# Optimization experiments

Hardware: AMD Instinct MI355X
Metric: run time of the kernel (lower is better)

## Reference

```python
import jax, jax.numpy as jnp
import numpy as np

B, S, T = 32, 128, 64
H = 512
VS = VT = 32000


def _lstm_cell(x, h, c, W, U, b):
    # Keras LSTM gate order: i, f, g(cell), o
    z = x @ W + h @ U + b
    i, f, g, o = jnp.split(z, 4, axis=-1)
    c = jax.nn.sigmoid(f) * c + jax.nn.sigmoid(i) * jnp.tanh(g)
    h = jax.nn.sigmoid(o) * jnp.tanh(c)
    return h, c


def _lstm_scan(xs, h0, c0, W, U, b):
    # xs: [S, B, D]
    def step(carry, x):
        h, c = _lstm_cell(x, carry[0], carry[1], W, U, b)
        return (h, c), h
    (hT, cT), hs = jax.lax.scan(step, (h0, c0), xs)
    return hs, hT, cT


def setup_inputs() -> dict:
    key = jax.random.key(0)
    ks = jax.random.split(key, 16)
    def n(k, shape, s=0.02):
        return (jax.random.normal(k, shape, jnp.float32) * s).astype(jnp.float32)
    return {
        "src": jax.random.randint(ks[0], (B, S), 0, VS, jnp.int32),
        "trg": jax.random.randint(ks[1], (B, T), 0, VT, jnp.int32),
        "E_src": n(ks[2], (VS, H)),
        "E_trg": n(ks[3], (VT, H)),
        "Wf": n(ks[4], (H, 4 * H)), "Uf": n(ks[5], (H, 4 * H)), "bf": jnp.zeros((4 * H,), jnp.float32),
        "Wb": n(ks[6], (H, 4 * H)), "Ub": n(ks[7], (H, 4 * H)), "bb": jnp.zeros((4 * H,), jnp.float32),
        "Wd": n(ks[8], (H, 4 * H)), "Ud": n(ks[9], (H, 4 * H)), "bd": jnp.zeros((4 * H,), jnp.float32),
        "fcW": n(ks[10], (2 * H, H)), "fcb": jnp.zeros((H,), jnp.float32),
        "clsW": n(ks[11], (2 * H, VT)), "clsb": jnp.zeros((VT,), jnp.float32),
    }


def reference(src, trg, E_src, E_trg, Wf, Uf, bf, Wb, Ub, bb, Wd, Ud, bd, fcW, fcb, clsW, clsb):
    Bn = src.shape[0]
    Hn = E_src.shape[1]
    # --- Encoder: bidirectional LSTM ---
    xs = E_src[src].transpose(1, 0, 2)          # [S, B, H]
    z0 = jnp.zeros((Bn, Hn), xs.dtype)
    hs_f, hf, cf = _lstm_scan(xs, z0, z0, Wf, Uf, bf)
    hs_b, hb, cb = _lstm_scan(xs[::-1], z0, z0, Wb, Ub, bb)
    src_hidden = jnp.concatenate([hs_f, hs_b[::-1]], axis=-1).transpose(1, 0, 2)  # [B, S, 2H]
    # --- shared fc projections (same Dense, 2H -> H) ---
    src_h = src_hidden @ fcW + fcb                                   # [B, S, H]
    prev_h = jnp.concatenate([hf, hb], axis=-1) @ fcW + fcb          # [B, H]
    prev_c = jnp.concatenate([cf, cb], axis=-1) @ fcW + fcb          # [B, H]
    neg = jnp.where(src == 0, jnp.float32(-1e9), jnp.float32(0.0))   # [B, S]
    # --- Decoder (teacher forcing): per-step LSTM cell + dot-product attention ---
    ys = E_trg[trg[:, :-1]].transpose(1, 0, 2)  # [T-1, B, H]

    def step(carry, x):
        h, c = _lstm_cell(x, carry[0], carry[1], Wd, Ud, bd)
        score = jnp.einsum('bh,bsh->bs', h, src_h) + neg
        attn = jax.nn.softmax(score, axis=-1)
        ws = jnp.einsum('bs,bsh->bh', attn, src_h)
        return (h, c), jnp.concatenate([ws, h], axis=-1)  # dec_state [B, 2H]

    _, dec = jax.lax.scan(step, (prev_h, prev_c), ys)     # [T-1, B, 2H]
    logits = dec.transpose(1, 0, 2) @ clsW + clsb          # [B, T-1, VT]
    return logits
```

## Files before the change

### kernel.cpp

```cpp
#include <hip/hip_runtime.h>
#include <hip/hip_bf16.h>
#include <stdint.h>
#include <string.h>

constexpr int cB = 32, cS = 128, cT = 64, cH = 512, cH4 = 2048, cVT = 32000, cTM1 = 63;

typedef __attribute__((ext_vector_type(8))) __bf16 bf16x8;
typedef __attribute__((ext_vector_type(4))) float f32x4;

__device__ __forceinline__ float sigm(float x) { return 1.0f / (1.0f + expf(-x)); }

__device__ __forceinline__ bf16x8 sc_load16(const __hip_bfloat16* p) {
  bf16x8 r;
  asm volatile("global_load_dwordx4 %0, %1, off sc0 sc1"
               : "=&v"(r) : "v"(p) : "memory");
  return r;
}
__device__ __forceinline__ unsigned sc_load4u(const __hip_bfloat16* p) {
  unsigned r;
  asm volatile("global_load_dword %0, %1, off sc0 sc1"
               : "=&v"(r) : "v"(p) : "memory");
  return r;
}
__device__ __forceinline__ void sc_store4(__hip_bfloat16* p, unsigned v) {
  asm volatile("global_store_dword %0, %1, off sc0 sc1"
               :: "v"(p), "v"(v) : "memory");
}
__device__ __forceinline__ void pl_store4(__hip_bfloat16* p, unsigned v) {
  asm volatile("global_store_dword %0, %1, off"
               :: "v"(p), "v"(v) : "memory");
}
__device__ __forceinline__ unsigned sc_loadu(const unsigned* p) {
  unsigned r;
  asm volatile("global_load_dword %0, %1, off sc0 sc1"
               : "=&v"(r) : "v"(p) : "memory");
  asm volatile("s_waitcnt vmcnt(0)" ::: "memory");
  return r;
}
__device__ __forceinline__ void sc_storeu(unsigned* p, unsigned v) {
  asm volatile("global_store_dword %0, %1, off sc0 sc1"
               :: "v"(p), "v"(v) : "memory");
}

__global__ __launch_bounds__(64) void k_init_bars(unsigned* p) {
  p[threadIdx.x] = 0u;
}

__global__ __launch_bounds__(128) void k_embed_src(const int* __restrict__ src,
                                                   const float* __restrict__ E,
                                                   __hip_bfloat16* __restrict__ xs_bf,
                                                   float* __restrict__ neg) {
  int sb = blockIdx.x;
  int s = sb >> 5, b = sb & 31;
  int tok = src[b * cS + s];
  float4 e = ((const float4*)(E + (size_t)tok * cH))[threadIdx.x];
  __hip_bfloat16* drow = xs_bf + (size_t)sb * cH + threadIdx.x * 4;
  drow[0] = __float2bfloat16(e.x); drow[1] = __float2bfloat16(e.y);
  drow[2] = __float2bfloat16(e.z); drow[3] = __float2bfloat16(e.w);
  if (threadIdx.x == 0) neg[b * cS + s] = (tok == 0) ? -1e9f : 0.0f;
}

__global__ __launch_bounds__(128) void k_embed_trg(const int* __restrict__ trg,
                                                   const float* __restrict__ E,
                                                   __hip_bfloat16* __restrict__ ys_bf) {
  int tb = blockIdx.x;
  int t = tb >> 5, b = tb & 31;
  int tok = trg[b * cT + t];
  float4 e = ((const float4*)(E + (size_t)tok * cH))[threadIdx.x];
  __hip_bfloat16* drow = ys_bf + (size_t)tb * cH + threadIdx.x * 4;
  drow[0] = __float2bfloat16(e.x); drow[1] = __float2bfloat16(e.y);
  drow[2] = __float2bfloat16(e.z); drow[3] = __float2bfloat16(e.w);
}

__device__ __forceinline__ void f2bT_tile(const float* __restrict__ src,
                                          __hip_bfloat16* __restrict__ dst,
                                          int K, int N, int gi, int bx, int by,
                                          float (*t)[33]) {
  int nt = bx * 32, kt = by * 32;
  int c = threadIdx.x & 31, r0 = threadIdx.x >> 5;
#pragma unroll
  for (int i = 0; i < 4; ++i) {
    int r = r0 + i * 8;
    t[r][c] = src[(size_t)(kt + r) * N + nt + c];
  }
  __syncthreads();
#pragma unroll
  for (int i = 0; i < 4; ++i) {
    int row = nt + r0 + i * 8;
    int pr = gi ? (((row & 511) << 2) | (row >> 9)) : row;
    dst[(size_t)pr * K + kt + c] = __float2bfloat16(t[c][r0 + i * 8]);
  }
  __syncthreads();
}

__device__ __forceinline__ void f2bT_tile512(const float* __restrict__ src,
                                             __hip_bfloat16* __restrict__ dst,
                                             int K, int N, int bx, int by,
                                             float (*t)[33]) {
  int nt = bx * 32, kt = by * 32;
  int c = threadIdx.x & 31, r0 = (threadIdx.x >> 5) & 15;
#pragma unroll
  for (int i = 0; i < 2; ++i) {
    int r = r0 + i * 16;
    t[r][c] = src[(size_t)(kt + r) * N + nt + c];
  }
  __syncthreads();
#pragma unroll
  for (int i = 0; i < 2; ++i) {
    int row = nt + r0 + i * 16;
    dst[(size_t)row * K + kt + c] = __float2bfloat16(t[c][r0 + i * 16]);
  }
  __syncthreads();
}

__global__ __launch_bounds__(256) void k_prep(
    const float* __restrict__ Wf, const float* __restrict__ Wb, const float* __restrict__ Wd,
    const float* __restrict__ Uf, const float* __restrict__ Ub, const float* __restrict__ Ud,
    const float* __restrict__ fcW,
    const float* __restrict__ bf, const float* __restrict__ bb, const float* __restrict__ bd,
    __hip_bfloat16* __restrict__ Wtfx, __hip_bfloat16* __restrict__ Wtbx,
    __hip_bfloat16* __restrict__ Wtdx,
    __hip_bfloat16* __restrict__ Utf, __hip_bfloat16* __restrict__ Utb,
    __hip_bfloat16* __restrict__ Utd,
    __hip_bfloat16* __restrict__ fcWt,
    float* __restrict__ bfx, float* __restrict__ bbx, float* __restrict__ bdx,
    __hip_bfloat16* __restrict__ ys_pad) {
  __shared__ float t[32][33];
  int id = blockIdx.x;
  if (id < 6144) {
    int grp = id >> 10, r = id & 1023;
    const float* s; __hip_bfloat16* d;
    switch (grp) {
      case 0: s = Wf; d = Wtfx; break;
      case 1: s = Wb; d = Wtbx; break;
      case 2: s = Wd; d = Wtdx; break;
      case 3: s = Uf; d = Utf; break;
      case 4: s = Ub; d = Utb; break;
      default: s = Ud; d = Utd; break;
    }
    f2bT_tile(s, d, 512, 2048, 1, r & 63, r >> 6, t);
  } else if (id < 6656) {
    int r = id - 6144;
    f2bT_tile(fcW, fcWt, 1024, 512, 0, r & 15, r >> 4, t);
  } else if (id < 6680) {
    int r = id - 6656;
    const float* s = (r < 8) ? bf : ((r < 16) ? bb : bd);
    float* d = (r < 8) ? bfx : ((r < 16) ? bbx : bdx);
    int i = (r & 7) * 256 + threadIdx.x;
    d[i] = s[(i & 3) * 512 + (i >> 2)];
  } else {
    int r = id - 6680;
    ys_pad[r * 256 + threadIdx.x] = __float2bfloat16(0.0f);
  }
}

__global__ __launch_bounds__(256) void k_bgemm(const __hip_bfloat16* __restrict__ A,
                                               const __hip_bfloat16* __restrict__ Bt,
                                               const float* __restrict__ bias,
                                               float* __restrict__ C,
                                               int M, int K, int N) {
  __shared__ __hip_bfloat16 As[128 * 64];
  __shared__ __hip_bfloat16 Bs[128 * 64];
  const int tid = threadIdx.x;
  const int lane = tid & 63;
  const int wave = tid >> 6;
  const int wr = wave >> 1, wc = wave & 1;
  const int bm = blockIdx.x * 128, bn = blockIdx.y * 128;

  f32x4 acc[4][4] = {};

  const int srow = lane >> 3;
  const int scol = (lane & 7) * 8;

  for (int kt = 0; kt < K; kt += 64) {
#pragma unroll
    for (int i = 0; i < 4; ++i) {
      int c = wave * 4 + i;
      const __hip_bfloat16* ga = A + (size_t)(bm + c * 8 + srow) * K + kt + scol;
      __builtin_amdgcn_global_load_lds(
          (const __attribute__((address_space(1))) uint32_t*)ga,
          (__attribute__((address_space(3))) uint32_t*)(As + c * 512), 16, 0, 0);
      const __hip_bfloat16* gb = Bt + (size_t)(bn + c * 8 + srow) * K + kt + scol;
      __builtin_amdgcn_global_load_lds(
          (const __attribute__((address_space(1))) uint32_t*)gb,
          (__attribute__((address_space(3))) uint32_t*)(Bs + c * 512), 16, 0, 0);
    }
    __syncthreads();

#pragma unroll
    for (int kk = 0; kk < 64; kk += 32) {
      const int ko = kk + (lane >> 4) * 8;
      bf16x8 a[4], b[4];
      const int ar = wr * 64 + (lane & 15);
#pragma unroll
      for (int m = 0; m < 4; ++m)
        a[m] = *(const bf16x8*)(As + (size_t)(ar + m * 16) * 64 + ko);
      const int br = wc * 64 + (lane & 15);
#pragma unroll
      for (int n = 0; n < 4; ++n)
        b[n] = *(const bf16x8*)(Bs + (size_t)(br + n * 16) * 64 + ko);
#pragma unroll
      for (int m = 0; m < 4; ++m)
#pragma unroll
        for (int n = 0; n < 4; ++n)
          acc[m][n] = __builtin_amdgcn_mfma_f32_16x16x32_bf16(a[m], b[n], acc[m][n], 0, 0, 0);
    }
    __syncthreads();
  }

#pragma unroll
  for (int m = 0; m < 4; ++m) {
    const int row0 = bm + wr * 64 + m * 16 + (lane >> 4) * 4;
#pragma unroll
    for (int n = 0; n < 4; ++n) {
      const int col = bn + wc * 64 + n * 16 + (lane & 15);
      const float bv = bias[col];
#pragma unroll
      for (int r = 0; r < 4; ++r) {
        const int row = row0 + r;
        if (row < M) C[(size_t)row * N + col] = acc[m][n][r] + bv;
      }
    }
  }
}

#define SLOT_BARRIER(SLOTS, NB, GEN)                                             \
  {                                                                              \
    asm volatile("s_waitcnt vmcnt(2)" ::: "memory");                             \
    __builtin_amdgcn_sched_barrier(0);                                           \
    __builtin_amdgcn_s_barrier();                                                \
    if (tid == 0) sc_storeu((SLOTS) + (NB), (unsigned)(GEN));                    \
    if (wv == 0) {                                                               \
      for (;;) {                                                                 \
        unsigned v = sc_loadu((SLOTS) + (lane & 15));                            \
        if (__all((lane >= 16) | (v >= (unsigned)(GEN)))) break;                 \
        __builtin_amdgcn_s_sleep(1);                                             \
      }                                                                          \
    }                                                                            \
    __builtin_amdgcn_s_barrier();                                                \
    __builtin_amdgcn_sched_barrier(0);                                           \
  }

#define ENC_STEP(T, ZI0, ZI1, ZO0, ZO1)                                          \
  {                                                                              \
    const int t = (T);                                                           \
    const int trow = dir ? (127 - t) : t;                                        \
    if (t > 0) {                                                                 \
      const __hip_bfloat16* hsrc = hcur + (size_t)((t + 1) & 1) * 16384;         \
      bf16x8 hr[4];                                                              \
      _Pragma("unroll")                                                          \
      for (int i = 0; i < 4; ++i) {                                              \
        int c = tid + i * 512;                                                   \
        hr[i] = sc_load16(hsrc + (size_t)c * 8);                                 \
      }                                                                          \
      asm volatile("s_waitcnt vmcnt(0)" ::: "memory");                           \
      __builtin_amdgcn_sched_barrier(0);                                         \
      _Pragma("unroll")                                                          \
      for (int i = 0; i < 4; ++i) {                                              \
        int c = tid + i * 512;                                                   \
        int r = c >> 6, cc = (c & 63) * 8;                                       \
        *(bf16x8*)&Hs[r][cc] = hr[i];                                            \
      }                                                                          \
      asm volatile("s_waitcnt lgkmcnt(0)" ::: "memory");                         \
      __builtin_amdgcn_s_barrier();                                              \
      __builtin_amdgcn_sched_barrier(0);                                         \
    }                                                                            \
    f32x4 acc0 = {}, acc1 = {};                                                  \
    if (t > 0) {                                                                 \
      _Pragma("unroll")                                                          \
      for (int kk = 0; kk < 16; ++kk) {                                          \
        bf16x8 h0v = *(const bf16x8*)&Hs[b0][kk * 32 + fq * 8];                  \
        bf16x8 h1v = *(const bf16x8*)&Hs[b1][kk * 32 + fq * 8];                  \
        acc0 = __builtin_amdgcn_mfma_f32_16x16x32_bf16(afrag[kk], h0v, acc0, 0, 0, 0); \
        acc1 = __builtin_amdgcn_mfma_f32_16x16x32_bf16(afrag[kk], h1v, acc1, 0, 0, 0); \
      }                                                                          \
    }                                                                            \
    {                                                                            \
      float zi = ZI0[0] + acc0[0], zf = ZI0[1] + acc0[1],                        \
            zg = ZI0[2] + acc0[2], zo = ZI0[3] + acc0[3];                        \
      cs0 = sigm(zf) * cs0 + sigm(zi) * tanhf(zg);                               \
      Ho[b0][jloc] = __float2bfloat16(sigm(zo) * tanhf(cs0));                    \
    }                                                                            \
    {                                                                            \
      float zi = ZI1[0] + acc1[0], zf = ZI1[1] + acc1[1],                        \
            zg = ZI1[2] + acc1[2], zo = ZI1[3] + acc1[3];                        \
      cs1 = sigm(zf) * cs1 + sigm(zi) * tanhf(zg);                               \
      Ho[b1][jloc] = __float2bfloat16(sigm(zo) * tanhf(cs1));                    \
    }                                                                            \
    asm volatile("s_waitcnt lgkmcnt(0)" ::: "memory");                           \
    __builtin_amdgcn_s_barrier();                                                \
    __builtin_amdgcn_sched_barrier(0);                                           \
    {                                                                            \
      unsigned v = *(const unsigned*)&Ho[bb][jp];                                \
      sc_store4(hcur + (size_t)(t & 1) * 16384 + (size_t)bb * 512 + nb * 32 + jp, v); \
      pl_store4(catb + ((size_t)(bb * 128 + trow)) * 1024 + dhalf + nb * 32 + jp, v); \
    }                                                                            \
    __builtin_amdgcn_sched_barrier(0);                                           \
    const int tn = (t < 127) ? t + 1 : 127;                                      \
    const int ntrow = dir ? (127 - tn) : tn;                                     \
    ZO0 = *(const f32x4*)(xW + ((size_t)(ntrow * 32 + b0)) * 2048 + zc);         \
    ZO1 = *(const f32x4*)(xW + ((size_t)(ntrow * 32 + b1)) * 2048 + zc);         \
    if (t < 127) SLOT_BARRIER(slots, nb, t + 1);                                 \
  }

__global__ __launch_bounds__(512, 1) void k_enc_mfma(
    const float* __restrict__ xWf, const float* __restrict__ xWb,
    const __hip_bfloat16* __restrict__ Utf, const __hip_bfloat16* __restrict__ Utb,
    __hip_bfloat16* __restrict__ catb,
    __hip_bfloat16* __restrict__ henc,
    float* __restrict__ cf, float* __restrict__ cb,
    unsigned* bars) {
  __shared__ __hip_bfloat16 Hs[32][520];
  __shared__ __hip_bfloat16 Ho[32][36];

  const int bid = blockIdx.x;
  const int dir = bid >> 4, nb = bid & 15;
  const int c0 = nb * 128;
  const float* xW = dir ? xWb : xWf;
  const __hip_bfloat16* Ut = dir ? Utb : Utf;
  const int dhalf = dir * 512;
  __hip_bfloat16* hcur = henc + (size_t)dir * 32768;
  float* cOut = dir ? cb : cf;
  unsigned* slots = bars + dir * 16;

  const int tid = threadIdx.x;
  const int lane = tid & 63;
  const int wv = tid >> 6;
  const int fr = lane & 15;
  const int fq = lane >> 4;

  bf16x8 afrag[16];
#pragma unroll
  for (int kk = 0; kk < 16; ++kk)
    afrag[kk] = *(const bf16x8*)(Ut + (size_t)(c0 + wv * 16 + fr) * 512 + kk * 32 + fq * 8);

  const int jglob = nb * 32 + wv * 4 + fq;
  const int jloc = wv * 4 + fq;
  const int b0 = fr, b1 = fr + 16;
  const int zc = c0 + wv * 16 + fq * 4;
  const int bb = tid >> 4, jp = (tid & 15) * 2;
  float cs0 = 0.f, cs1 = 0.f;

  const int trow0 = dir ? 127 : 0;
  f32x4 zA0 = *(const f32x4*)(xW + ((size_t)(trow0 * 32 + b0)) * 2048 + zc);
  f32x4 zA1 = *(const f32x4*)(xW + ((size_t)(trow0 * 32 + b1)) * 2048 + zc);
  f32x4 zB0, zB1;

  for (int it = 0; it < 64; ++it) {
    ENC_STEP(2 * it, zA0, zA1, zB0, zB1);
    ENC_STEP(2 * it + 1, zB0, zB1, zA0, zA1);
  }
  cOut[(size_t)b0 * 512 + jglob] = cs0;
  cOut[(size_t)b1 * 512 + jglob] = cs1;
}

__device__ void attn_one(const float* __restrict__ src_h, const float* __restrict__ neg,
                         __hip_bfloat16* __restrict__ decb, int b, int t,
                         float* hv, float* sc, float* red) {
  const int tx = threadIdx.x;
  __hip_bfloat16* drow = decb + ((size_t)b * cTM1 + t) * 1024;
  if (tx < 256) {
    unsigned u = sc_load4u(drow + 512 + tx * 2);
    asm volatile("s_waitcnt vmcnt(0)" ::: "memory");
    hv[tx * 2] = __uint_as_float(u << 16);
    hv[tx * 2 + 1] = __uint_as_float(u & 0xffff0000u);
  }
  __syncthreads();
  {
    int s = tx >> 2, q = tx & 3;
    const float4* sr = (const float4*)(src_h + ((size_t)b * cS + s) * cH + q * 128);
    const float4* hh = (const float4*)(hv + q * 128);
    float acc = 0.f;
#pragma unroll 8
    for (int k = 0; k < 32; ++k) {
      float4 v = sr[k], h4 = hh[k];
      acc += v.x * h4.x + v.y * h4.y + v.z * h4.z + v.w * h4.w;
    }
    acc += __shfl_xor(acc, 1);
    acc += __shfl_xor(acc, 2);
    if (q == 0) {
      float s0 = acc + neg[b * cS + s];
      sc[s] = s0;
      red[s] = s0;
    }
  }
  __syncthreads();
  for (int off = 64; off >= 1; off >>= 1) {
    if (tx < off) red[tx] = fmaxf(red[tx], red[tx + off]);
    __syncthreads();
  }
  float mx = red[0];
  __syncthreads();
  float e = 0.f;
  if (tx < cS) { e = expf(sc[tx] - mx); red[tx] = e; }
  __syncthreads();
  for (int off = 64; off >= 1; off >>= 1) {
    if (tx < off) red[tx] += red[tx + off];
    __syncthreads();
  }
  float inv = 1.0f / red[0];
  __syncthreads();
  if (tx < cS) sc[tx] = e * inv;
  __syncthreads();
  {
    float a = 0.f;
    const float* sr = src_h + (size_t)b * cS * cH + tx;
    for (int s = 0; s < cS; ++s) a += sc[s] * sr[(size_t)s * cH];
    drow[tx] = __float2bfloat16(a);
  }
}

#define DEC_STEP(T, ZI0, ZI1, ZO0, ZO1)                                          \
  {                                                                              \
    const int t = (T);                                                           \
    if (t == 0) {                                                                \
      const float4* ph4 = (const float4*)prev_h;                                 \
      _Pragma("unroll")                                                          \
      for (int i = 0; i < 8; ++i) {                                              \
        int c = tid + i * 512;                                                   \
        float4 v = ph4[c];                                                       \
        int r = c >> 7, c4 = (c & 127) * 4;                                      \
        Hs[r][c4 + 0] = __float2bfloat16(v.x);                                   \
        Hs[r][c4 + 1] = __float2bfloat16(v.y);                                   \
        Hs[r][c4 + 2] = __float2bfloat16(v.z);                                   \
        Hs[r][c4 + 3] = __float2bfloat16(v.w);                                   \
      }                                                                          \
    } else {                                                                     \
      const __hip_bfloat16* hsrc = hdec + (size_t)((t + 1) & 1) * 16384;         \
      bf16x8 hr[4];                                                              \
      _Pragma("unroll")                                                          \
      for (int i = 0; i < 4; ++i) {                                              \
        int c = tid + i * 512;                                                   \
        hr[i] = sc_load16(hsrc + (size_t)c * 8);                                 \
      }                                                                          \
      asm volatile("s_waitcnt vmcnt(0)" ::: "memory");                           \
      __builtin_amdgcn_sched_barrier(0);                                         \
      _Pragma("unroll")                                                          \
      for (int i = 0; i < 4; ++i) {                                              \
        int c = tid + i * 512;                                                   \
        int r = c >> 6, cc = (c & 63) * 8;                                       \
        *(bf16x8*)&Hs[r][cc] = hr[i];                                            \
      }                                                                          \
    }                                                                            \
    asm volatile("s_waitcnt lgkmcnt(0)" ::: "memory");                           \
    __builtin_amdgcn_s_barrier();                                                \
    __builtin_amdgcn_sched_barrier(0);                                           \
    f32x4 acc0 = {}, acc1 = {};                                                  \
    _Pragma("unroll")                                                            \
    for (int kk = 0; kk < 16; ++kk) {                                            \
      bf16x8 h0v = *(const bf16x8*)&Hs[b0][kk * 32 + fq * 8];                    \
      bf16x8 h1v = *(const bf16x8*)&Hs[b1][kk * 32 + fq * 8];                    \
      acc0 = __builtin_amdgcn_mfma_f32_16x16x32_bf16(afrag[kk], h0v, acc0, 0, 0, 0); \
      acc1 = __builtin_amdgcn_mfma_f32_16x16x32_bf16(afrag[kk], h1v, acc1, 0, 0, 0); \
    }                                                                            \
    {                                                                            \
      float zi = ZI0[0] + acc0[0], zf = ZI0[1] + acc0[1],                        \
            zg = ZI0[2] + acc0[2], zo = ZI0[3] + acc0[3];                        \
      cs0 = sigm(zf) * cs0 + sigm(zi) * tanhf(zg);                               \
      Ho[b0][jloc] = __float2bfloat16(sigm(zo) * tanhf(cs0));                    \
    }                                                                            \
    {                                                                            \
      float zi = ZI1[0] + acc1[0], zf = ZI1[1] + acc1[1],                        \
            zg = ZI1[2] + acc1[2], zo = ZI1[3] + acc1[3];                        \
      cs1 = sigm(zf) * cs1 + sigm(zi) * tanhf(zg);                               \
      Ho[b1][jloc] = __float2bfloat16(sigm(zo) * tanhf(cs1));                    \
    }                                                                            \
    asm volatile("s_waitcnt lgkmcnt(0)" ::: "memory");                           \
    __builtin_amdgcn_s_barrier();                                                \
    __builtin_amdgcn_sched_barrier(0);                                           \
    {                                                                            \
      unsigned v = *(const unsigned*)&Ho[bb][jp];                                \
      sc_store4(hdec + (size_t)(t & 1) * 16384 + (size_t)bb * 512 + nb * 32 + jp, v); \
      sc_store4(decb + ((size_t)bb * cTM1 + t) * 1024 + 512 + nb * 32 + jp, v);  \
    }                                                                            \
    __builtin_amdgcn_sched_barrier(0);                                           \
    const int tn = (t < cTM1 - 1) ? t + 1 : cTM1 - 1;                            \
    ZO0 = *(const f32x4*)(yW + ((size_t)(tn * 32 + b0)) * 2048 + zc);            \
    ZO1 = *(const f32x4*)(yW + ((size_t)(tn * 32 + b1)) * 2048 + zc);            \
    if (t < cTM1 - 1) SLOT_BARRIER(slots, nb, t + 1);                            \
  }

__global__ __launch_bounds__(512, 1) void k_dec_mfma(
    const float* __restrict__ yW, const __hip_bfloat16* __restrict__ Utd,
    const float* __restrict__ prev_h, const float* __restrict__ prev_c,
    __hip_bfloat16* __restrict__ hdec, __hip_bfloat16* __restrict__ decb,
    const float* __restrict__ clsW, __hip_bfloat16* __restrict__ clsWt,
    const float* __restrict__ src_h, const float* __restrict__ neg,
    unsigned* slots) {
  __shared__ __hip_bfloat16 Hs[32][520];
  __shared__ __hip_bfloat16 Ho[32][36];
  __shared__ float tcv[32][33];
  __shared__ float hv_sh[512];
  __shared__ float sc_sh[128];
  __shared__ float red_sh[128];

  const int tid = threadIdx.x;
  const int lane = tid & 63;
  const int wv = tid >> 6;

  if (blockIdx.x >= 16) {
    const int sidx = blockIdx.x - 16;
    for (int tile = sidx; tile < 32000; tile += 240) {
      f2bT_tile512(clsW, clsWt, 1024, 32000, tile % 1000, tile / 1000, tcv);
    }
    unsigned waited = 0;
    for (int i = sidx; i < 2016; i += 240) {
      int t = i >> 5, b = i & 31;
      unsigned need = (unsigned)(t + 1);
      if (need > waited) {
        if (wv == 0) {
          for (;;) {
            unsigned v = sc_loadu(slots + (lane & 15));
            if (__all((lane >= 16) | (v >= need))) break;
            __builtin_amdgcn_s_sleep(4);
          }
        }
        __syncthreads();
        waited = need;
      }
      attn_one(src_h, neg, decb, b, t, hv_sh, sc_sh, red_sh);
    }
    return;
  }

  const int nb = blockIdx.x;
  const int c0 = nb * 128;
  const int fr = lane & 15;
  const int fq = lane >> 4;

  bf16x8 afrag[16];
#pragma unroll
  for (int kk = 0; kk < 16; ++kk)
    afrag[kk] = *(const bf16x8*)(Utd + (size_t)(c0 + wv * 16 + fr) * 512 + kk * 32 + fq * 8);

  const int jglob = nb * 32 + wv * 4 + fq;
  const int jloc = wv * 4 + fq;
  const int b0 = fr, b1 = fr + 16;
  const int zc = c0 + wv * 16 + fq * 4;
  const int bb = tid >> 4, jp = (tid & 15) * 2;
  float cs0 = prev_c[(size_t)b0 * 512 + jglob];
  float cs1 = prev_c[(size_t)b1 * 512 + jglob];

  f32x4 zA0 = *(const f32x4*)(yW + ((size_t)b0) * 2048 + zc);
  f32x4 zA1 = *(const f32x4*)(yW + ((size_t)b1) * 2048 + zc);
  f32x4 zB0, zB1;

  for (int it = 0; it < 31; ++it) {
    DEC_STEP(2 * it, zA0, zA1, zB0, zB1);
    DEC_STEP(2 * it + 1, zB0, zB1, zA0, zA1);
  }
  DEC_STEP(62, zA0, zA1, zB0, zB1);
  asm volatile("s_waitcnt vmcnt(0)" ::: "memory");
  __builtin_amdgcn_s_barrier();
  if (tid == 0) sc_storeu(slots + nb, (unsigned)cTM1);
}

__global__ __launch_bounds__(128) void k_cat_tail(const float* __restrict__ cf,
                                                  const float* __restrict__ cb,
                                                  __hip_bfloat16* __restrict__ cat) {
  int r = 4096 + blockIdx.x;
  int tid = threadIdx.x;
  __hip_bfloat16* drow = cat + (size_t)r * 1024 + tid * 8;
  if (r >= 4160) {
    bf16x8 zv = {};
    *(bf16x8*)drow = zv;
    return;
  }
  if (r < 4128) {
    int b = r - 4096;
    const __hip_bfloat16* pf = cat + ((size_t)(b * 128 + 127)) * 1024;
    const __hip_bfloat16* pb = cat + ((size_t)(b * 128 + 0)) * 1024 + 512;
    const __hip_bfloat16* s8 = (tid < 64) ? (pf + tid * 8) : (pb + (tid - 64) * 8);
    *(bf16x8*)drow = *(const bf16x8*)s8;
  } else {
    int b = r - 4128;
    const float* s8 = (tid < 64) ? (cf + (size_t)b * 512 + tid * 8)
                                 : (cb + (size_t)b * 512 + (tid - 64) * 8);
    bf16x8 v;
#pragma unroll
    for (int i = 0; i < 8; ++i) v[i] = (__bf16)s8[i];
    *(bf16x8*)drow = v;
  }
}

extern "C" void kernel_launch(void* const* d_in, const int* in_sizes, int n_in,
                              void* d_out, int out_size, void* d_ws, size_t ws_size,
                              hipStream_t stream) {
  const int* src = (const int*)d_in[0];
  const int* trg = (const int*)d_in[1];
  const float* E_src = (const float*)d_in[2];
  const float* E_trg = (const float*)d_in[3];
  const float* Wf = (const float*)d_in[4];
  const float* Uf = (const float*)d_in[5];
  const float* bf = (const float*)d_in[6];
  const float* Wb = (const float*)d_in[7];
  const float* Ub = (const float*)d_in[8];
  const float* bb = (const float*)d_in[9];
  const float* Wd = (const float*)d_in[10];
  const float* Ud = (const float*)d_in[11];
  const float* bd = (const float*)d_in[12];
  const float* fcW = (const float*)d_in[13];
  const float* fcb = (const float*)d_in[14];
  const float* clsW = (const float*)d_in[15];
  const float* clsb = (const float*)d_in[16];
  float* out = (float*)d_out;
  float* ws = (float*)d_ws;

  float* xWf = ws;
  float* xWb = ws + 8388608;
  float* yW = ws + 16777216;
  float* cf = ws + 23003136;
  float* cb = ws + 23019520;
  float* neg = ws + 23035904;
  float* fco = ws + 23040000;
  __hip_bfloat16* decb = (__hip_bfloat16*)(ws + 25169920);
  __hip_bfloat16* Utd = (__hip_bfloat16*)(ws + 26218496);
  __hip_bfloat16* henc = (__hip_bfloat16*)(ws + 26742784);
  __hip_bfloat16* hdec = (__hip_bfloat16*)(ws + 26808320);
  unsigned* bars = (unsigned*)(ws + 26841088);
  float* pool = ws + 26841152;

  __hip_bfloat16* xs_bf = (__hip_bfloat16*)pool;
  __hip_bfloat16* ys_bf = (__hip_bfloat16*)(pool + 1048576);
  __hip_bfloat16* Utf = (__hip_bfloat16*)(pool + 1572864);
  __hip_bfloat16* Utb = (__hip_bfloat16*)(pool + 2097152);
  __hip_bfloat16* Wtfx = (__hip_bfloat16*)(pool + 2621440);
  __hip_bfloat16* Wtbx = (__hip_bfloat16*)(pool + 3145728);
  __hip_bfloat16* Wtdx = (__hip_bfloat16*)(pool + 3670016);
  float* bfx = pool + 4194304;
  float* bbx = pool + 4196352;
  float* bdx = pool + 4198400;
  __hip_bfloat16* fcWt = (__hip_bfloat16*)(pool + 4200448);
  __hip_bfloat16* cat_bf = (__hip_bfloat16*)(pool + 4462592);
  __hip_bfloat16* clsWt = (__hip_bfloat16*)xWf;

  k_embed_src<<<4096, 128, 0, stream>>>(src, E_src, xs_bf, neg);
  k_embed_trg<<<2016, 128, 0, stream>>>(trg, E_trg, ys_bf);
  k_prep<<<6744, 256, 0, stream>>>(Wf, Wb, Wd, Uf, Ub, Ud, fcW, bf, bb, bd,
                                   Wtfx, Wtbx, Wtdx, Utf, Utb, Utd, fcWt,
                                   bfx, bbx, bdx, ys_bf + (size_t)2016 * 512);

  k_bgemm<<<dim3(32, 16), 256, 0, stream>>>(xs_bf, Wtfx, bfx, xWf, 4096, 512, 2048);
  k_bgemm<<<dim3(32, 16), 256, 0, stream>>>(xs_bf, Wtbx, bbx, xWb, 4096, 512, 2048);
  k_bgemm<<<dim3(16, 16), 256, 0, stream>>>(ys_bf, Wtdx, bdx, yW, 2016, 512, 2048);

  k_init_bars<<<1, 64, 0, stream>>>(bars);
  k_enc_mfma<<<32, 512, 0, stream>>>(xWf, xWb, Utf, Utb, cat_bf, henc, cf, cb, bars);

  k_cat_tail<<<128, 128, 0, stream>>>(cf, cb, cat_bf);
  k_bgemm<<<dim3(33, 4), 256, 0, stream>>>(cat_bf, fcWt, fcb, fco, 4160, 1024, 512);

  const float* prev_h = fco + (size_t)4096 * 512;
  const float* prev_c = fco + (size_t)4128 * 512;
  k_dec_mfma<<<256, 512, 0, stream>>>(yW, Utd, prev_h, prev_c, hdec, decb,
                                      clsW, clsWt, fco, neg, bars + 32);

  k_bgemm<<<dim3(16, 250), 256, 0, stream>>>(decb, clsWt, clsb, out, 2016, 1024, 32000);
}
```

Baseline: 1.174 ms.

## Fuse prep kernels and overlap decoder input GEMM with encoder recurrence

Folds the embedding gathers, barrier init and cat padding into the single prep kernel, and merges the forward and backward input GEMMs into one launch using a z grid dimension. The decoder input projection (yW GEMM) now runs on 224 extra blocks of the encoder recurrence kernel, so it uses CUs that sit idle during the sequential LSTM loop. The encoder writes its final hidden and cell states straight into the concat buffer, which removes the cat_tail kernel and the cf/cb buffers. This cuts launch count and hides the GEMM, at the risk of the extra blocks competing with the latency-bound recurrence blocks for CUs or bandwidth, and of spin barriers depending on co-residency.

```diff
diff --git a/kernel.cpp b/kernel.cpp
--- a/kernel.cpp
+++ b/kernel.cpp
@@ -42,36 +42,6 @@
                :: "v"(p), "v"(v) : "memory");
 }
 
-__global__ __launch_bounds__(64) void k_init_bars(unsigned* p) {
-  p[threadIdx.x] = 0u;
-}
-
-__global__ __launch_bounds__(128) void k_embed_src(const int* __restrict__ src,
-                                                   const float* __restrict__ E,
-                                                   __hip_bfloat16* __restrict__ xs_bf,
-                                                   float* __restrict__ neg) {
-  int sb = blockIdx.x;
-  int s = sb >> 5, b = sb & 31;
-  int tok = src[b * cS + s];
-  float4 e = ((const float4*)(E + (size_t)tok * cH))[threadIdx.x];
-  __hip_bfloat16* drow = xs_bf + (size_t)sb * cH + threadIdx.x * 4;
-  drow[0] = __float2bfloat16(e.x); drow[1] = __float2bfloat16(e.y);
-  drow[2] = __float2bfloat16(e.z); drow[3] = __float2bfloat16(e.w);
-  if (threadIdx.x == 0) neg[b * cS + s] = (tok == 0) ? -1e9f : 0.0f;
-}
-
-__global__ __launch_bounds__(128) void k_embed_trg(const int* __restrict__ trg,
-                                                   const float* __restrict__ E,
-                                                   __hip_bfloat16* __restrict__ ys_bf) {
-  int tb = blockIdx.x;
-  int t = tb >> 5, b = tb & 31;
-  int tok = trg[b * cT + t];
-  float4 e = ((const float4*)(E + (size_t)tok * cH))[threadIdx.x];
-  __hip_bfloat16* drow = ys_bf + (size_t)tb * cH + threadIdx.x * 4;
-  drow[0] = __float2bfloat16(e.x); drow[1] = __float2bfloat16(e.y);
-  drow[2] = __float2bfloat16(e.z); drow[3] = __float2bfloat16(e.w);
-}
-
 __device__ __forceinline__ void f2bT_tile(const float* __restrict__ src,
                                           __hip_bfloat16* __restrict__ dst,
                                           int K, int N, int gi, int bx, int by,
@@ -118,15 +88,20 @@
     const float* __restrict__ Uf, const float* __restrict__ Ub, const float* __restrict__ Ud,
     const float* __restrict__ fcW,
     const float* __restrict__ bf, const float* __restrict__ bb, const float* __restrict__ bd,
+    const int* __restrict__ src, const int* __restrict__ trg,
+    const float* __restrict__ E_src, const float* __restrict__ E_trg,
     __hip_bfloat16* __restrict__ Wtfx, __hip_bfloat16* __restrict__ Wtbx,
     __hip_bfloat16* __restrict__ Wtdx,
     __hip_bfloat16* __restrict__ Utf, __hip_bfloat16* __restrict__ Utb,
     __hip_bfloat16* __restrict__ Utd,
     __hip_bfloat16* __restrict__ fcWt,
     float* __restrict__ bfx, float* __restrict__ bbx, float* __restrict__ bdx,
-    __hip_bfloat16* __restrict__ ys_pad) {
+    __hip_bfloat16* __restrict__ xs_bf, __hip_bfloat16* __restrict__ ys_bf,
+    float* __restrict__ neg, __hip_bfloat16* __restrict__ catb,
+    unsigned* __restrict__ bars) {
   __shared__ float t[32][33];
   int id = blockIdx.x;
+  int tid = threadIdx.x;
   if (id < 6144) {
     int grp = id >> 10, r = id & 1023;
     const float* s; __hip_bfloat16* d;
@@ -146,11 +121,39 @@
     int r = id - 6656;
     const float* s = (r < 8) ? bf : ((r < 16) ? bb : bd);
     float* d = (r < 8) ? bfx : ((r < 16) ? bbx : bdx);
-    int i = (r & 7) * 256 + threadIdx.x;
+    int i = (r & 7) * 256 + tid;
     d[i] = s[(i & 3) * 512 + (i >> 2)];
+  } else if (id < 6744) {
+    int r = id - 6680;
+    ys_bf[(size_t)2016 * 512 + r * 256 + tid] = __float2bfloat16(0.0f);
+  } else if (id < 6776) {
+    int r = id - 6744;
+    __hip_bfloat16* d = catb + (size_t)4160 * 1024 + (size_t)r * 2048 + tid * 8;
+    bf16x8 zv = {};
+    *(bf16x8*)d = zv;
+  } else if (id < 8824) {
+    int r = id - 6776;
+    int half = tid >> 7, sb = 2 * r + half;
+    int s = sb >> 5, b = sb & 31;
+    int tok = src[b * cS + s];
+    int cg = tid & 127;
+    float4 e = ((const float4*)(E_src + (size_t)tok * cH))[cg];
+    __hip_bfloat16* drow = xs_bf + (size_t)sb * cH + cg * 4;
+    drow[0] = __float2bfloat16(e.x); drow[1] = __float2bfloat16(e.y);
+    drow[2] = __float2bfloat16(e.z); drow[3] = __float2bfloat16(e.w);
+    if (cg == 0) neg[b * cS + s] = (tok == 0) ? -1e9f : 0.0f;
+  } else if (id < 9832) {
+    int r = id - 8824;
+    int half = tid >> 7, tb = 2 * r + half;
+    int tt = tb >> 5, b = tb & 31;
+    int tok = trg[b * cT + tt];
+    int cg = tid & 127;
+    float4 e = ((const float4*)(E_trg + (size_t)tok * cH))[cg];
+    __hip_bfloat16* drow = ys_bf + (size_t)tb * cH + cg * 4;
+    drow[0] = __float2bfloat16(e.x); drow[1] = __float2bfloat16(e.y);
+    drow[2] = __float2bfloat16(e.z); drow[3] = __float2bfloat16(e.w);
   } else {
-    int r = id - 6680;
-    ys_pad[r * 256 + threadIdx.x] = __float2bfloat16(0.0f);
+    if (tid < 64) bars[tid] = 0u;
   }
 }
 
@@ -208,6 +211,78 @@
     __syncthreads();
   }
 
+#pragma unroll
+  for (int m = 0; m < 4; ++m) {
+    const int row0 = bm + wr * 64 + m * 16 + (lane >> 4) * 4;
+#pragma unroll
+    for (int n = 0; n < 4; ++n) {
+      const int col = bn + wc * 64 + n * 16 + (lane & 15);
+      const float bv = bias[col];
+#pragma unroll
+      for (int r = 0; r < 4; ++r) {
+        const int row = row0 + r;
+        if (row < M) C[(size_t)row * N + col] = acc[m][n][r] + bv;
+      }
+    }
+  }
+}
+
+__global__ __launch_bounds__(256) void k_bgemm2(
+    const __hip_bfloat16* __restrict__ A,
+    const __hip_bfloat16* __restrict__ Bt0, const __hip_bfloat16* __restrict__ Bt1,
+    const float* __restrict__ bias0, const float* __restrict__ bias1,
+    float* __restrict__ C0, float* __restrict__ C1,
+    int M, int K, int N) {
+  const __hip_bfloat16* Bt = blockIdx.z ? Bt1 : Bt0;
+  const float* bias = blockIdx.z ? bias1 : bias0;
+  float* C = blockIdx.z ? C1 : C0;
+
+  __shared__ __hip_bfloat16 As[128 * 64];
+  __shared__ __hip_bfloat16 Bs[128 * 64];
+  const int tid = threadIdx.x;
+  const int lane = tid & 63;
+  const int wave = tid >> 6;
+  const int wr = wave >> 1, wc = wave & 1;
+  const int bm = blockIdx.x * 128, bn = blockIdx.y * 128;
+
+  f32x4 acc[4][4] = {};
+  const int srow = lane >> 3;
+  const int scol = (lane & 7) * 8;
+
+  for (int kt = 0; kt < K; kt += 64) {
+#pragma unroll
+    for (int i = 0; i < 4; ++i) {
+      int c = wave * 4 + i;
+      const __hip_bfloat16* ga = A + (size_t)(bm + c * 8 + srow) * K + kt + scol;
+      __builtin_amdgcn_global_load_lds(
+          (const __attribute__((address_space(1))) uint32_t*)ga,
+          (__attribute__((address_space(3))) uint32_t*)(As + c * 512), 16, 0, 0);
+      const __hip_bfloat16* gb = Bt + (size_t)(bn + c * 8 + srow) * K + kt + scol;
+      __builtin_amdgcn_global_load_lds(
+          (const __attribute__((address_space(1))) uint32_t*)gb,
+          (__attribute__((address_space(3))) uint32_t*)(Bs + c * 512), 16, 0, 0);
+    }
+    __syncthreads();
+#pragma unroll
+    for (int kk = 0; kk < 64; kk += 32) {
+      const int ko = kk + (lane >> 4) * 8;
+      bf16x8 a[4], b[4];
+      const int ar = wr * 64 + (lane & 15);
+#pragma unroll
+      for (int m = 0; m < 4; ++m)
+        a[m] = *(const bf16x8*)(As + (size_t)(ar + m * 16) * 64 + ko);
+      const int br = wc * 64 + (lane & 15);
+#pragma unroll
+      for (int n = 0; n < 4; ++n)
+        b[n] = *(const bf16x8*)(Bs + (size_t)(br + n * 16) * 64 + ko);
+#pragma unroll
+      for (int m = 0; m < 4; ++m)
+#pragma unroll
+        for (int n = 0; n < 4; ++n)
+          acc[m][n] = __builtin_amdgcn_mfma_f32_16x16x32_bf16(a[m], b[n], acc[m][n], 0, 0, 0);
+    }
+    __syncthreads();
+  }
 #pragma unroll
   for (int m = 0; m < 4; ++m) {
     const int row0 = bm + wr * 64 + m * 16 + (lane >> 4) * 4;
@@ -308,10 +383,72 @@
     const __hip_bfloat16* __restrict__ Utf, const __hip_bfloat16* __restrict__ Utb,
     __hip_bfloat16* __restrict__ catb,
     __hip_bfloat16* __restrict__ henc,
-    float* __restrict__ cf, float* __restrict__ cb,
-    unsigned* bars) {
+    unsigned* bars,
+    const __hip_bfloat16* __restrict__ ys_bf, const __hip_bfloat16* __restrict__ Wtdx,
+    const float* __restrict__ bdx, float* __restrict__ yW) {
   __shared__ __hip_bfloat16 Hs[32][520];
   __shared__ __hip_bfloat16 Ho[32][36];
+  __shared__ __hip_bfloat16 As[8192];
+  __shared__ __hip_bfloat16 Bs[8192];
+
+  const int tid = threadIdx.x;
+  const int lane = tid & 63;
+  const int wv = tid >> 6;
+
+  if (blockIdx.x >= 32) {
+    const int sidx = blockIdx.x - 32;
+    const int wr = wv >> 2, wc = wv & 3;
+    const int fr = lane & 15, fq = lane >> 4;
+    for (int tile = sidx; tile < 256; tile += 224) {
+      int bm = (tile & 15) * 128, bn = (tile >> 4) * 128;
+      f32x4 acc[4][2] = {};
+      for (int kt = 0; kt < 512; kt += 64) {
+#pragma unroll
+        for (int i = 0; i < 2; ++i) {
+          int ch = wv * 2 + i;
+          const __hip_bfloat16* ga = ys_bf + (size_t)(bm + ch * 8 + (lane >> 3)) * 512 + kt + (lane & 7) * 8;
+          __builtin_amdgcn_global_load_lds(
+              (const __attribute__((address_space(1))) uint32_t*)ga,
+              (__attribute__((address_space(3))) uint32_t*)(As + ch * 512), 16, 0, 0);
+          const __hip_bfloat16* gb = Wtdx + (size_t)(bn + ch * 8 + (lane >> 3)) * 512 + kt + (lane & 7) * 8;
+          __builtin_amdgcn_global_load_lds(
+              (const __attribute__((address_space(1))) uint32_t*)gb,
+              (__attribute__((address_space(3))) uint32_t*)(Bs + ch * 512), 16, 0, 0);
+        }
+        __syncthreads();
+#pragma unroll
+        for (int kk = 0; kk < 64; kk += 32) {
+          const int ko = kk + fq * 8;
+          bf16x8 a[4], b[2];
+#pragma unroll
+          for (int m = 0; m < 4; ++m)
+            a[m] = *(const bf16x8*)(As + (size_t)(wr * 64 + m * 16 + fr) * 64 + ko);
+#pragma unroll
+          for (int n = 0; n < 2; ++n)
+            b[n] = *(const bf16x8*)(Bs + (size_t)(wc * 32 + n * 16 + fr) * 64 + ko);
+#pragma unroll
+          for (int m = 0; m < 4; ++m)
+#pragma unroll
+            for (int n = 0; n < 2; ++n)
+              acc[m][n] = __builtin_amdgcn_mfma_f32_16x16x32_bf16(a[m], b[n], acc[m][n], 0, 0, 0);
+        }
+        __syncthreads();
+      }
+#pragma unroll
+      for (int m = 0; m < 4; ++m) {
+        const int row0 = bm + wr * 64 + m * 16 + fq * 4;
+#pragma unroll
+        for (int n = 0; n < 2; ++n) {
+          const int col = bn + wc * 32 + n * 16 + fr;
+          const float bv = bdx[col];
+#pragma unroll
+          for (int r = 0; r < 4; ++r)
+            yW[(size_t)(row0 + r) * 2048 + col] = acc[m][n][r] + bv;
+        }
+      }
+    }
+    return;
+  }
 
   const int bid = blockIdx.x;
   const int dir = bid >> 4, nb = bid & 15;
@@ -320,12 +457,8 @@
   const __hip_bfloat16* Ut = dir ? Utb : Utf;
   const int dhalf = dir * 512;
   __hip_bfloat16* hcur = henc + (size_t)dir * 32768;
-  float* cOut = dir ? cb : cf;
   unsigned* slots = bars + dir * 16;
 
-  const int tid = threadIdx.x;
-  const int lane = tid & 63;
-  const int wv = tid >> 6;
   const int fr = lane & 15;
   const int fq = lane >> 4;
 
@@ -334,7 +467,6 @@
   for (int kk = 0; kk < 16; ++kk)
     afrag[kk] = *(const bf16x8*)(Ut + (size_t)(c0 + wv * 16 + fr) * 512 + kk * 32 + fq * 8);
 
-  const int jglob = nb * 32 + wv * 4 + fq;
   const int jloc = wv * 4 + fq;
   const int b0 = fr, b1 = fr + 16;
   const int zc = c0 + wv * 16 + fq * 4;
@@ -350,8 +482,20 @@
     ENC_STEP(2 * it, zA0, zA1, zB0, zB1);
     ENC_STEP(2 * it + 1, zB0, zB1, zA0, zA1);
   }
-  cOut[(size_t)b0 * 512 + jglob] = cs0;
-  cOut[(size_t)b1 * 512 + jglob] = cs1;
+
+  {
+    unsigned v = *(const unsigned*)&Ho[bb][jp];
+    pl_store4(catb + (size_t)(4096 + bb) * 1024 + dhalf + nb * 32 + jp, v);
+  }
+  __syncthreads();
+  Ho[b0][jloc] = __float2bfloat16(cs0);
+  Ho[b1][jloc] = __float2bfloat16(cs1);
+  asm volatile("s_waitcnt lgkmcnt(0)" ::: "memory");
+  __builtin_amdgcn_s_barrier();
+  {
+    unsigned v = *(const unsigned*)&Ho[bb][jp];
+    pl_store4(catb + (size_t)(4128 + bb) * 1024 + dhalf + nb * 32 + jp, v);
+  }
 }
 
 __device__ void attn_one(const float* __restrict__ src_h, const float* __restrict__ neg,
@@ -555,34 +699,6 @@
   if (tid == 0) sc_storeu(slots + nb, (unsigned)cTM1);
 }
 
-__global__ __launch_bounds__(128) void k_cat_tail(const float* __restrict__ cf,
-                                                  const float* __restrict__ cb,
-                                                  __hip_bfloat16* __restrict__ cat) {
-  int r = 4096 + blockIdx.x;
-  int tid = threadIdx.x;
-  __hip_bfloat16* drow = cat + (size_t)r * 1024 + tid * 8;
-  if (r >= 4160) {
-    bf16x8 zv = {};
-    *(bf16x8*)drow = zv;
-    return;
-  }
-  if (r < 4128) {
-    int b = r - 4096;
-    const __hip_bfloat16* pf = cat + ((size_t)(b * 128 + 127)) * 1024;
-    const __hip_bfloat16* pb = cat + ((size_t)(b * 128 + 0)) * 1024 + 512;
-    const __hip_bfloat16* s8 = (tid < 64) ? (pf + tid * 8) : (pb + (tid - 64) * 8);
-    *(bf16x8*)drow = *(const bf16x8*)s8;
-  } else {
-    int b = r - 4128;
-    const float* s8 = (tid < 64) ? (cf + (size_t)b * 512 + tid * 8)
-                                 : (cb + (size_t)b * 512 + (tid - 64) * 8);
-    bf16x8 v;
-#pragma unroll
-    for (int i = 0; i < 8; ++i) v[i] = (__bf16)s8[i];
-    *(bf16x8*)drow = v;
-  }
-}
-
 extern "C" void kernel_launch(void* const* d_in, const int* in_sizes, int n_in,
                               void* d_out, int out_size, void* d_ws, size_t ws_size,
                               hipStream_t stream) {
@@ -609,8 +725,6 @@
   float* xWf = ws;
   float* xWb = ws + 8388608;
   float* yW = ws + 16777216;
-  float* cf = ws + 23003136;
-  float* cb = ws + 23019520;
   float* neg = ws + 23035904;
   float* fco = ws + 23040000;
   __hip_bfloat16* decb = (__hip_bfloat16*)(ws + 25169920);
@@ -634,20 +748,17 @@
   __hip_bfloat16* cat_bf = (__hip_bfloat16*)(pool + 4462592);
   __hip_bfloat16* clsWt = (__hip_bfloat16*)xWf;
 
-  k_embed_src<<<4096, 128, 0, stream>>>(src, E_src, xs_bf, neg);
-  k_embed_trg<<<2016, 128, 0, stream>>>(trg, E_trg, ys_bf);
-  k_prep<<<6744, 256, 0, stream>>>(Wf, Wb, Wd, Uf, Ub, Ud, fcW, bf, bb, bd,
+  k_prep<<<9833, 256, 0, stream>>>(Wf, Wb, Wd, Uf, Ub, Ud, fcW, bf, bb, bd,
+                                   src, trg, E_src, E_trg,
                                    Wtfx, Wtbx, Wtdx, Utf, Utb, Utd, fcWt,
-                                   bfx, bbx, bdx, ys_bf + (size_t)2016 * 512);
-
-  k_bgemm<<<dim3(32, 16), 256, 0, stream>>>(xs_bf, Wtfx, bfx, xWf, 4096, 512, 2048);
-  k_bgemm<<<dim3(32, 16), 256, 0, stream>>>(xs_bf, Wtbx, bbx, xWb, 4096, 512, 2048);
-  k_bgemm<<<dim3(16, 16), 256, 0, stream>>>(ys_bf, Wtdx, bdx, yW, 2016, 512, 2048);
-
-  k_init_bars<<<1, 64, 0, stream>>>(bars);
-  k_enc_mfma<<<32, 512, 0, stream>>>(xWf, xWb, Utf, Utb, cat_bf, henc, cf, cb, bars);
-
-  k_cat_tail<<<128, 128, 0, stream>>>(cf, cb, cat_bf);
+                                   bfx, bbx, bdx, xs_bf, ys_bf, neg, cat_bf, bars);
+
+  k_bgemm2<<<dim3(32, 16, 2), 256, 0, stream>>>(xs_bf, Wtfx, Wtbx, bfx, bbx,
+                                                xWf, xWb, 4096, 512, 2048);
+
+  k_enc_mfma<<<256, 512, 0, stream>>>(xWf, xWb, Utf, Utb, cat_bf, henc, bars,
+                                      ys_bf, Wtdx, bdx, yW);
+
   k_bgemm<<<dim3(33, 4), 256, 0, stream>>>(cat_bf, fcWt, fcb, fco, 4160, 1024, 512);
 
   const float* prev_h = fco + (size_t)4096 * 512;
```

After: 1.146 ms (median of 2 runs). -2.4%, faster.
